# Performance work log

Measured on AMD Instinct MI355X. Metric: run time of the kernel, lower is better.

The kernel has to match this reference:

```python
import jax, jax.numpy as jnp
import numpy as np

N_NODES = 2048
EMBED = 256
STATE = 128
HID = 256
N_ACT = 256
TEAMS = 8
PAIR_F = 14


def setup_inputs() -> dict:
    key = jax.random.key(0)
    ks = jax.random.split(key, 12)
    B, T = 16, 32
    node_embeddings = jax.random.normal(ks[0], (N_NODES, EMBED), jnp.float32)
    states = jax.random.normal(ks[1], (B, T, STATE), jnp.float32)
    pair_features = jax.random.normal(ks[2], (B, T, N_ACT, PAIR_F), jnp.float32)
    proc_action_indices = jax.random.randint(ks[3], (N_ACT,), 0, N_NODES)
    in_dim = EMBED * 4 + PAIR_F
    s = lambda k, sh, fan: jax.random.normal(k, sh, jnp.float32) / np.sqrt(fan)
    return {
        "node_embeddings": node_embeddings,
        "states": states,
        "pair_features": pair_features,
        "proc_action_indices": proc_action_indices,
        "team_table": jax.random.normal(ks[4], (TEAMS, EMBED), jnp.float32),
        "Ws": s(ks[5], (STATE, EMBED), STATE),
        "bs": jnp.zeros((EMBED,), jnp.float32),
        "W1": s(ks[6], (in_dim, HID), in_dim),
        "b1": jnp.zeros((HID,), jnp.float32),
        "W2": s(ks[7], (HID, HID), HID),
        "b2": jnp.zeros((HID,), jnp.float32),
        "W3": s(ks[8], (HID, 1), HID),
        "b3": jnp.zeros((1,), jnp.float32),
    }


def reference(node_embeddings, states, pair_features, proc_action_indices,
              team_table, Ws, bs, W1, b1, W2, b2, W3, b3):
    B, T, A, F = pair_features.shape
    team_ids = jnp.arange(A) % TEAMS  # registered buffer
    # [A, E] gathered / per-action embeddings
    proc_emb = node_embeddings[proc_action_indices]          # [A, E]
    team_emb = team_table[team_ids]                          # [A, E]
    global_emb = jnp.mean(node_embeddings, axis=0)           # [E]
    state_emb = jax.nn.relu(states @ Ws + bs)                # [B, T, E]
    # broadcast + concat -> [B, T, A, 4E + F]
    bT = (B, T, A)
    scorer_input = jnp.concatenate([
        jnp.broadcast_to(proc_emb[None, None], bT + (proc_emb.shape[-1],)),
        jnp.broadcast_to(team_emb[None, None], bT + (team_emb.shape[-1],)),
        jnp.broadcast_to(global_emb[None, None, None], bT + (global_emb.shape[-1],)),
        jnp.broadcast_to(state_emb[:, :, None], bT + (state_emb.shape[-1],)),
        pair_features,
    ], axis=-1)
    h = jax.nn.relu(scorer_input @ W1 + b1)
    h = jax.nn.relu(h @ W2 + b2)
    scores = (h @ W3 + b3)[..., 0]  # [B, T, A]
    return scores[:, :, None, :]    # [B, T, 1, A]
```

## Files before the change

kernel.cpp:

```cpp
#include <hip/hip_runtime.h>
#include <hip/hip_bf16.h>

#define N_NODES 2048
#define EMBED 256
#define STATE 128
#define HID 256
#define N_ACT 256
#define TEAMS 8
#define PAIR_F 14
#define BT_TOTAL 512
#define M_TOTAL (BT_TOTAL * N_ACT)

typedef _Float16 f16_t;
typedef _Float16 f16x8 __attribute__((ext_vector_type(8)));
typedef _Float16 f16x4 __attribute__((ext_vector_type(4)));
typedef float f32x4 __attribute__((ext_vector_type(4)));

__device__ __forceinline__ size_t reord_idx(int k, int n, int KB) {
    return (size_t)(((n >> 4) * KB + (k >> 5)) * 4 + ((k >> 3) & 3)) * 128 +
           (size_t)(n & 15) * 8 + (k & 7);
}

__device__ __forceinline__ size_t par_idx(int a, int n) {
    return (size_t)(a >> 4) * 4096 + (size_t)(n >> 2) * 64 + (a & 15) * 4 + (n & 3);
}

__global__ void k_prep(const float* __restrict__ ne, const int* __restrict__ idx,
                       const float* __restrict__ team, const float* __restrict__ states,
                       const float* __restrict__ Ws, const float* __restrict__ W1,
                       const float* __restrict__ W2, float* __restrict__ gpart,
                       f16_t* __restrict__ vecs, f16_t* __restrict__ W1abT,
                       f16_t* __restrict__ W1dT, f16_t* __restrict__ WsT,
                       f16_t* __restrict__ W2s, f16_t* __restrict__ w1pt,
                       f16_t* __restrict__ states_h) {
    int bid = blockIdx.x;
    if (bid < 64) {
        int t = threadIdx.x;
        float s = 0.f;
        const float* base = ne + (size_t)bid * 32 * EMBED + t;
#pragma unroll
        for (int i = 0; i < 32; ++i) s += base[(size_t)i * EMBED];
        gpart[bid * EMBED + t] = s;
        return;
    }
    int i = (bid - 64) * 256 + threadIdx.x;
    if (i < 131072) {
        int a = i >> 9, e = i & 511;
        float v = (e < 256) ? ne[(size_t)idx[a] * EMBED + e]
                            : team[(a % TEAMS) * EMBED + (e - 256)];
        vecs[i] = (f16_t)v;
        return;
    }
    i -= 131072;
    if (i < 131072) {
        int k = i >> 8, n = i & 255;
        W1abT[reord_idx(k, n, 16)] = (f16_t)W1[(size_t)k * HID + n];
        return;
    }
    i -= 131072;
    if (i < 65536) {
        int k = i >> 8, n = i & 255;
        W1dT[reord_idx(k, n, 8)] = (f16_t)W1[(size_t)(768 + k) * HID + n];
        return;
    }
    i -= 65536;
    if (i < 32768) {
        int k = i >> 8, n = i & 255;
        WsT[reord_idx(k, n, 4)] = (f16_t)Ws[(size_t)k * EMBED + n];
        return;
    }
    i -= 32768;
    if (i < 65536) {
        int k = i >> 8, n = i & 255;
        W2s[reord_idx(k, n, 8)] = (f16_t)W2[(size_t)k * HID + n];
        return;
    }
    i -= 65536;
    if (i < 8192) {
        int k = i >> 8, n = i & 255;
        float v = (k < PAIR_F) ? W1[(size_t)(1024 + k) * HID + n] : 0.f;
        w1pt[reord_idx(k, n, 1)] = (f16_t)v;
        return;
    }
    i -= 8192;
    if (i < 65536) states_h[i] = (f16_t)states[i];
}

__global__ __launch_bounds__(256, 4) void k_pp(
    const f16_t* __restrict__ states_h, const f16_t* __restrict__ WsT,
    const float* __restrict__ bs, const f16_t* __restrict__ W1dT,
    const f16_t* __restrict__ vecs, const f16_t* __restrict__ W1abT,
    const float* __restrict__ W1, const float* __restrict__ b1,
    const float* __restrict__ gpart, f16_t* __restrict__ paR,
    f16_t* __restrict__ pbt_h) {
    __shared__ __align__(16) f16_t se[64 * 256];
    __shared__ float gm[256];
    const int tid = threadIdx.x;
    const int wid = tid >> 6, lane = tid & 63;
    const int c = lane & 15, q = lane >> 4;
    int bid = blockIdx.x;

    if (bid >= 8) {
        int b = bid - 8;
        const int m0 = (b >> 2) * 64, n0 = (b & 3) * 64;
        const int n = n0 + wid * 16 + c;
        const int g = n >> 4;
        f32x4 acc[4] = {f32x4{0,0,0,0}, f32x4{0,0,0,0}, f32x4{0,0,0,0}, f32x4{0,0,0,0}};
        for (int ks = 0; ks < 16; ++ks) {
            f16x8 bf = *(const f16x8*)(W1abT + (size_t)((g * 16 + ks) * 4 + q) * 128 + c * 8);
#pragma unroll
            for (int mi = 0; mi < 4; ++mi) {
                f16x8 af = *(const f16x8*)(vecs + (size_t)(m0 + mi * 16 + c) * 512 + ks * 32 + q * 8);
                acc[mi] = __builtin_amdgcn_mfma_f32_16x16x32_f16(af, bf, acc[mi], 0, 0, 0);
            }
        }
        {
            float s = 0.f;
#pragma unroll 8
            for (int p = 0; p < 64; ++p) s += gpart[p * EMBED + tid];
            gm[tid] = s * (1.0f / N_NODES);
        }
        __syncthreads();
        float cvec = 0.f;
#pragma unroll 8
        for (int e = 0; e < 256; ++e)
            cvec = fmaf(gm[e], W1[(size_t)(512 + e) * HID + n], cvec);
        cvec += b1[n];
#pragma unroll
        for (int mi = 0; mi < 4; ++mi)
#pragma unroll
            for (int j = 0; j < 4; ++j) {
                int a = m0 + mi * 16 + q * 4 + j;
                paR[par_idx(a, n)] = (f16_t)(acc[mi][j] + cvec);
            }
        return;
    }

    const int bt0 = bid * 64;
    f32x4 acc[4][4];
#pragma unroll
    for (int mi = 0; mi < 4; ++mi)
#pragma unroll
        for (int ni = 0; ni < 4; ++ni) acc[mi][ni] = f32x4{0, 0, 0, 0};
#pragma unroll
    for (int ks = 0; ks < 4; ++ks) {
        f16x8 bh[4];
#pragma unroll
        for (int ni = 0; ni < 4; ++ni) {
            int g = wid * 4 + ni;
            bh[ni] = *(const f16x8*)(WsT + (size_t)((g * 4 + ks) * 4 + q) * 128 + c * 8);
        }
#pragma unroll
        for (int mi = 0; mi < 4; ++mi) {
            f16x8 af = *(const f16x8*)(states_h + (size_t)(bt0 + mi * 16 + c) * STATE + ks * 32 + q * 8);
#pragma unroll
            for (int ni = 0; ni < 4; ++ni)
                acc[mi][ni] = __builtin_amdgcn_mfma_f32_16x16x32_f16(af, bh[ni], acc[mi][ni], 0, 0, 0);
        }
    }
#pragma unroll
    for (int mi = 0; mi < 4; ++mi)
#pragma unroll
        for (int ni = 0; ni < 4; ++ni) {
            float bsv = bs[wid * 64 + ni * 16 + c];
#pragma unroll
            for (int j = 0; j < 4; ++j) {
                int m = mi * 16 + q * 4 + j;
                int n = wid * 64 + ni * 16 + c;
                se[m * 256 + (n ^ ((m & 7) << 3))] = (f16_t)fmaxf(acc[mi][ni][j] + bsv, 0.f);
            }
        }
#pragma unroll
    for (int mi = 0; mi < 4; ++mi)
#pragma unroll
        for (int ni = 0; ni < 4; ++ni) acc[mi][ni] = f32x4{0, 0, 0, 0};
    __syncthreads();
#pragma unroll
    for (int ks = 0; ks < 8; ++ks) {
        f16x8 bh[4];
#pragma unroll
        for (int ni = 0; ni < 4; ++ni) {
            int g = wid * 4 + ni;
            bh[ni] = *(const f16x8*)(W1dT + (size_t)((g * 8 + ks) * 4 + q) * 128 + c * 8);
        }
#pragma unroll
        for (int mi = 0; mi < 4; ++mi) {
            int m = mi * 16 + c;
            f16x8 ah = *(const f16x8*)(&se[m * 256 + ((ks * 32 + q * 8) ^ ((m & 7) << 3))]);
#pragma unroll
            for (int ni = 0; ni < 4; ++ni)
                acc[mi][ni] = __builtin_amdgcn_mfma_f32_16x16x32_f16(ah, bh[ni], acc[mi][ni], 0, 0, 0);
        }
    }
#pragma unroll
    for (int mi = 0; mi < 4; ++mi)
#pragma unroll
        for (int ni = 0; ni < 4; ++ni)
#pragma unroll
            for (int j = 0; j < 4; ++j)
                pbt_h[(size_t)(bt0 + mi * 16 + q * 4 + j) * HID + wid * 64 + ni * 16 + c] =
                    (f16_t)acc[mi][ni][j];
}

__global__ __launch_bounds__(256, 4) void k_main(
    const float* __restrict__ pf, const f16_t* __restrict__ paR,
    const f16_t* __restrict__ pbt, const f16_t* __restrict__ w2s,
    const f16_t* __restrict__ w1pt, const float* __restrict__ b2,
    const float* __restrict__ W3, const float* __restrict__ b3,
    float* __restrict__ out) {
    __shared__ __align__(16) f16_t Ah[64 * 256];
    __shared__ float red[4][64];

    const int tid = threadIdx.x;
    const int wc = tid >> 6, lane = tid & 63;
    const int c = lane & 15, q = lane >> 4;

    const int r0 = blockIdx.x * 64;
    const int bt = r0 >> 8;
    const int a0 = r0 & 255;

    f32x4 acc[16];
#pragma unroll
    for (int i = 0; i < 16; ++i) acc[i] = f32x4{0, 0, 0, 0};

    f16x8 af[4];
#pragma unroll
    for (int nf = 0; nf < 4; ++nf) {
        int g = wc * 4 + nf;
        af[nf] = *(const f16x8*)(w1pt + (size_t)(g * 4 + q) * 128 + c * 8);
    }
#pragma unroll
    for (int mf = 0; mf < 4; ++mf) {
        int m = mf * 16 + c;
        const float* row = pf + (size_t)(r0 + m) * PAIR_F;
        float2 v01{0, 0}, v23{0, 0}, v45{0, 0}, v67{0, 0};
        if (q == 0) {
            v01 = *(const float2*)(row);
            v23 = *(const float2*)(row + 2);
            v45 = *(const float2*)(row + 4);
            v67 = *(const float2*)(row + 6);
        } else if (q == 1) {
            v01 = *(const float2*)(row + 8);
            v23 = *(const float2*)(row + 10);
            v45 = *(const float2*)(row + 12);
        }
        f16x8 bf;
        bf[0] = (f16_t)v01.x; bf[1] = (f16_t)v01.y;
        bf[2] = (f16_t)v23.x; bf[3] = (f16_t)v23.y;
        bf[4] = (f16_t)v45.x; bf[5] = (f16_t)v45.y;
        bf[6] = (f16_t)v67.x; bf[7] = (f16_t)v67.y;
#pragma unroll
        for (int nf = 0; nf < 4; ++nf)
            acc[nf * 4 + mf] = __builtin_amdgcn_mfma_f32_16x16x32_f16(af[nf], bf, acc[nf * 4 + mf], 0, 0, 0);
    }

#pragma unroll
    for (int nf = 0; nf < 4; ++nf) {
        int n0 = wc * 64 + nf * 16 + q * 4;
        f16x4 pbtv = *(const f16x4*)(pbt + (size_t)bt * HID + n0);
#pragma unroll
        for (int mf = 0; mf < 4; ++mf) {
            int m = mf * 16 + c;
            f16x4 pav = *(const f16x4*)(paR + (size_t)((a0 >> 4) + mf) * 4096 +
                                        (size_t)(n0 >> 2) * 64 + c * 4);
            f16x4 hv;
#pragma unroll
            for (int j = 0; j < 4; ++j) {
                float h = acc[nf * 4 + mf][j] + (float)pav[j] + (float)pbtv[j];
                hv[j] = (f16_t)fmaxf(h, 0.f);
            }
            *(f16x4*)(&Ah[m * 256 + (n0 ^ ((m & 7) << 3))]) = hv;
        }
    }

#pragma unroll
    for (int i = 0; i < 16; ++i) acc[i] = f32x4{0, 0, 0, 0};

    __syncthreads();

#pragma unroll
    for (int ks = 0; ks < 8; ++ks) {
        f16x8 bh[4];
#pragma unroll
        for (int ni = 0; ni < 4; ++ni) {
            int g = wc * 4 + ni;
            bh[ni] = *(const f16x8*)(w2s + (size_t)((g * 8 + ks) * 4 + q) * 128 + c * 8);
        }
#pragma unroll
        for (int mi = 0; mi < 4; ++mi) {
            int m = mi * 16 + c;
            int kx = (ks * 32 + q * 8) ^ ((m & 7) << 3);
            f16x8 ah = *(const f16x8*)(&Ah[m * 256 + kx]);
#pragma unroll
            for (int ni = 0; ni < 4; ++ni)
                acc[mi * 4 + ni] = __builtin_amdgcn_mfma_f32_16x16x32_f16(ah, bh[ni], acc[mi * 4 + ni], 0, 0, 0);
        }
    }

    float p[4][4];
#pragma unroll
    for (int mi = 0; mi < 4; ++mi)
#pragma unroll
        for (int j = 0; j < 4; ++j) p[mi][j] = 0.f;
#pragma unroll
    for (int ni = 0; ni < 4; ++ni) {
        int n = wc * 64 + ni * 16 + c;
        float b2v = b2[n];
        float w3v = W3[n];
#pragma unroll
        for (int mi = 0; mi < 4; ++mi)
#pragma unroll
            for (int j = 0; j < 4; ++j)
                p[mi][j] = fmaf(fmaxf(acc[mi * 4 + ni][j] + b2v, 0.f), w3v, p[mi][j]);
    }
#pragma unroll
    for (int off = 1; off < 16; off <<= 1)
#pragma unroll
        for (int mi = 0; mi < 4; ++mi)
#pragma unroll
            for (int j = 0; j < 4; ++j) p[mi][j] += __shfl_xor(p[mi][j], off, 64);

    if (c == 0) {
#pragma unroll
        for (int mi = 0; mi < 4; ++mi)
#pragma unroll
            for (int j = 0; j < 4; ++j) red[wc][mi * 16 + q * 4 + j] = p[mi][j];
    }
    __syncthreads();

    if (tid < 64) {
        out[(size_t)r0 + tid] = red[0][tid] + red[1][tid] + red[2][tid] + red[3][tid] + b3[0];
    }
}

extern "C" void kernel_launch(void* const* d_in, const int* in_sizes, int n_in,
                              void* d_out, int out_size, void* d_ws, size_t ws_size,
                              hipStream_t stream) {
    (void)in_sizes; (void)n_in; (void)out_size; (void)ws_size;
    const float* ne     = (const float*)d_in[0];
    const float* states = (const float*)d_in[1];
    const float* pf     = (const float*)d_in[2];
    const int*   idx    = (const int*)d_in[3];
    const float* team   = (const float*)d_in[4];
    const float* Ws     = (const float*)d_in[5];
    const float* bs     = (const float*)d_in[6];
    const float* W1     = (const float*)d_in[7];
    const float* b1     = (const float*)d_in[8];
    const float* W2     = (const float*)d_in[9];
    const float* b2     = (const float*)d_in[10];
    const float* W3     = (const float*)d_in[11];
    const float* b3     = (const float*)d_in[12];
    float* out = (float*)d_out;

    char* ws = (char*)d_ws;
    float* gpart    = (float*)(ws + 0);
    f16_t* vecs     = (f16_t*)(ws + 65536);
    f16_t* W1abT    = (f16_t*)(ws + 327680);
    f16_t* W1dT     = (f16_t*)(ws + 589824);
    f16_t* WsT      = (f16_t*)(ws + 720896);
    f16_t* W2s      = (f16_t*)(ws + 786432);
    f16_t* w1pt     = (f16_t*)(ws + 917504);
    f16_t* states_h = (f16_t*)(ws + 933888);
    f16_t* paR      = (f16_t*)(ws + 1064960);
    f16_t* pbt_h    = (f16_t*)(ws + 1196032);

    k_prep<<<64 + 1952, 256, 0, stream>>>(ne, idx, team, states, Ws, W1, W2,
                                          gpart, vecs, W1abT, W1dT, WsT, W2s, w1pt, states_h);
    k_pp<<<24, 256, 0, stream>>>(states_h, WsT, bs, W1dT, vecs, W1abT, W1, b1,
                                 gpart, paR, pbt_h);
    k_main<<<M_TOTAL / 64, 256, 0, stream>>>(pf, paR, pbt_h, W2s, w1pt, b2, W3, b3, out);
}
```

Before: 52.98 us.

## Split global-mean into own kernel, MFMA the mean projection, stage pair features in LDS

The global-mean column sums move into a separate small kernel. k_prep then finishes the mean as fp16 and converts the W1 global-embedding block, so k_pp computes the constant term with MFMA instead of a serial 256-step scalar dot product per thread. k_main loads the block's pair features with coalesced float4 loads into shared memory and double-buffers the W2 fragment loads across k-steps. The costs are an extra kernel launch, an extra barrier in k_main, and the mean projection now running in fp16.

```diff
diff --git a/kernel.cpp b/kernel.cpp
--- a/kernel.cpp
+++ b/kernel.cpp
@@ -25,25 +25,26 @@
     return (size_t)(a >> 4) * 4096 + (size_t)(n >> 2) * 64 + (a & 15) * 4 + (n & 3);
 }
 
+__global__ void k_cs(const float* __restrict__ ne, float* __restrict__ gpart) {
+    int b = blockIdx.x;
+    int t = threadIdx.x;
+    float s = 0.f;
+    const float* base = ne + (size_t)b * 32 * EMBED + t;
+#pragma unroll
+    for (int i = 0; i < 32; ++i) s += base[(size_t)i * EMBED];
+    gpart[b * EMBED + t] = s;
+}
+
 __global__ void k_prep(const float* __restrict__ ne, const int* __restrict__ idx,
                        const float* __restrict__ team, const float* __restrict__ states,
                        const float* __restrict__ Ws, const float* __restrict__ W1,
-                       const float* __restrict__ W2, float* __restrict__ gpart,
+                       const float* __restrict__ W2, const float* __restrict__ gpart,
                        f16_t* __restrict__ vecs, f16_t* __restrict__ W1abT,
-                       f16_t* __restrict__ W1dT, f16_t* __restrict__ WsT,
-                       f16_t* __restrict__ W2s, f16_t* __restrict__ w1pt,
-                       f16_t* __restrict__ states_h) {
-    int bid = blockIdx.x;
-    if (bid < 64) {
-        int t = threadIdx.x;
-        float s = 0.f;
-        const float* base = ne + (size_t)bid * 32 * EMBED + t;
-#pragma unroll
-        for (int i = 0; i < 32; ++i) s += base[(size_t)i * EMBED];
-        gpart[bid * EMBED + t] = s;
-        return;
-    }
-    int i = (bid - 64) * 256 + threadIdx.x;
+                       f16_t* __restrict__ W1cT, f16_t* __restrict__ W1dT,
+                       f16_t* __restrict__ WsT, f16_t* __restrict__ W2s,
+                       f16_t* __restrict__ w1pt, f16_t* __restrict__ states_h,
+                       f16_t* __restrict__ gm_h) {
+    int i = blockIdx.x * 256 + threadIdx.x;
     if (i < 131072) {
         int a = i >> 9, e = i & 511;
         float v = (e < 256) ? ne[(size_t)idx[a] * EMBED + e]
@@ -60,6 +61,12 @@
     i -= 131072;
     if (i < 65536) {
         int k = i >> 8, n = i & 255;
+        W1cT[reord_idx(k, n, 8)] = (f16_t)W1[(size_t)(512 + k) * HID + n];
+        return;
+    }
+    i -= 65536;
+    if (i < 65536) {
+        int k = i >> 8, n = i & 255;
         W1dT[reord_idx(k, n, 8)] = (f16_t)W1[(size_t)(768 + k) * HID + n];
         return;
     }
@@ -83,18 +90,24 @@
         return;
     }
     i -= 8192;
-    if (i < 65536) states_h[i] = (f16_t)states[i];
+    if (i < 65536) { states_h[i] = (f16_t)states[i]; return; }
+    i -= 65536;
+    if (i < 256) {
+        float s = 0.f;
+#pragma unroll 8
+        for (int p = 0; p < 64; ++p) s += gpart[p * EMBED + i];
+        gm_h[i] = (f16_t)(s * (1.0f / N_NODES));
+    }
 }
 
 __global__ __launch_bounds__(256, 4) void k_pp(
     const f16_t* __restrict__ states_h, const f16_t* __restrict__ WsT,
     const float* __restrict__ bs, const f16_t* __restrict__ W1dT,
     const f16_t* __restrict__ vecs, const f16_t* __restrict__ W1abT,
-    const float* __restrict__ W1, const float* __restrict__ b1,
-    const float* __restrict__ gpart, f16_t* __restrict__ paR,
+    const f16_t* __restrict__ W1cT, const f16_t* __restrict__ gm_h,
+    const float* __restrict__ b1, f16_t* __restrict__ paR,
     f16_t* __restrict__ pbt_h) {
     __shared__ __align__(16) f16_t se[64 * 256];
-    __shared__ float gm[256];
     const int tid = threadIdx.x;
     const int wid = tid >> 6, lane = tid & 63;
     const int c = lane & 15, q = lane >> 4;
@@ -114,24 +127,21 @@
                 acc[mi] = __builtin_amdgcn_mfma_f32_16x16x32_f16(af, bf, acc[mi], 0, 0, 0);
             }
         }
-        {
-            float s = 0.f;
-#pragma unroll 8
-            for (int p = 0; p < 64; ++p) s += gpart[p * EMBED + tid];
-            gm[tid] = s * (1.0f / N_NODES);
-        }
-        __syncthreads();
-        float cvec = 0.f;
-#pragma unroll 8
-        for (int e = 0; e < 256; ++e)
-            cvec = fmaf(gm[e], W1[(size_t)(512 + e) * HID + n], cvec);
-        cvec += b1[n];
+#pragma unroll
+        for (int ks = 0; ks < 8; ++ks) {
+            f16x8 bf = *(const f16x8*)(W1cT + (size_t)((g * 8 + ks) * 4 + q) * 128 + c * 8);
+            f16x8 af = *(const f16x8*)(gm_h + ks * 32 + q * 8);
+#pragma unroll
+            for (int mi = 0; mi < 4; ++mi)
+                acc[mi] = __builtin_amdgcn_mfma_f32_16x16x32_f16(af, bf, acc[mi], 0, 0, 0);
+        }
+        float b1v = b1[n];
 #pragma unroll
         for (int mi = 0; mi < 4; ++mi)
 #pragma unroll
             for (int j = 0; j < 4; ++j) {
                 int a = m0 + mi * 16 + q * 4 + j;
-                paR[par_idx(a, n)] = (f16_t)(acc[mi][j] + cvec);
+                paR[par_idx(a, n)] = (f16_t)(acc[mi][j] + b1v);
             }
         return;
     }
@@ -209,6 +219,7 @@
     const float* __restrict__ W3, const float* __restrict__ b3,
     float* __restrict__ out) {
     __shared__ __align__(16) f16_t Ah[64 * 256];
+    __shared__ __align__(16) float pfs[64 * PAIR_F];
     __shared__ float red[4][64];
 
     const int tid = threadIdx.x;
@@ -219,6 +230,11 @@
     const int bt = r0 >> 8;
     const int a0 = r0 & 255;
 
+    if (tid < 224) {
+        const float4 v = ((const float4*)(pf + (size_t)r0 * PAIR_F))[tid];
+        *(float4*)&pfs[tid * 4] = v;
+    }
+
     f32x4 acc[16];
 #pragma unroll
     for (int i = 0; i < 16; ++i) acc[i] = f32x4{0, 0, 0, 0};
@@ -229,26 +245,19 @@
         int g = wc * 4 + nf;
         af[nf] = *(const f16x8*)(w1pt + (size_t)(g * 4 + q) * 128 + c * 8);
     }
+
+    __syncthreads();
+
 #pragma unroll
     for (int mf = 0; mf < 4; ++mf) {
         int m = mf * 16 + c;
-        const float* row = pf + (size_t)(r0 + m) * PAIR_F;
-        float2 v01{0, 0}, v23{0, 0}, v45{0, 0}, v67{0, 0};
-        if (q == 0) {
-            v01 = *(const float2*)(row);
-            v23 = *(const float2*)(row + 2);
-            v45 = *(const float2*)(row + 4);
-            v67 = *(const float2*)(row + 6);
-        } else if (q == 1) {
-            v01 = *(const float2*)(row + 8);
-            v23 = *(const float2*)(row + 10);
-            v45 = *(const float2*)(row + 12);
-        }
         f16x8 bf;
-        bf[0] = (f16_t)v01.x; bf[1] = (f16_t)v01.y;
-        bf[2] = (f16_t)v23.x; bf[3] = (f16_t)v23.y;
-        bf[4] = (f16_t)v45.x; bf[5] = (f16_t)v45.y;
-        bf[6] = (f16_t)v67.x; bf[7] = (f16_t)v67.y;
+#pragma unroll
+        for (int j = 0; j < 8; ++j) {
+            int k = q * 8 + j;
+            float v = (q < 2 && k < PAIR_F) ? pfs[m * PAIR_F + k] : 0.f;
+            bf[j] = (f16_t)v;
+        }
 #pragma unroll
         for (int nf = 0; nf < 4; ++nf)
             acc[nf * 4 + mf] = __builtin_amdgcn_mfma_f32_16x16x32_f16(af[nf], bf, acc[nf * 4 + mf], 0, 0, 0);
@@ -278,13 +287,21 @@
 
     __syncthreads();
 
+    f16x8 bh[4];
+#pragma unroll
+    for (int ni = 0; ni < 4; ++ni) {
+        int g = wc * 4 + ni;
+        bh[ni] = *(const f16x8*)(w2s + (size_t)((g * 8 + 0) * 4 + q) * 128 + c * 8);
+    }
 #pragma unroll
     for (int ks = 0; ks < 8; ++ks) {
-        f16x8 bh[4];
-#pragma unroll
-        for (int ni = 0; ni < 4; ++ni) {
-            int g = wc * 4 + ni;
-            bh[ni] = *(const f16x8*)(w2s + (size_t)((g * 8 + ks) * 4 + q) * 128 + c * 8);
+        f16x8 bhn[4];
+        if (ks < 7) {
+#pragma unroll
+            for (int ni = 0; ni < 4; ++ni) {
+                int g = wc * 4 + ni;
+                bhn[ni] = *(const f16x8*)(w2s + (size_t)((g * 8 + ks + 1) * 4 + q) * 128 + c * 8);
+            }
         }
 #pragma unroll
         for (int mi = 0; mi < 4; ++mi) {
@@ -295,6 +312,8 @@
             for (int ni = 0; ni < 4; ++ni)
                 acc[mi * 4 + ni] = __builtin_amdgcn_mfma_f32_16x16x32_f16(ah, bh[ni], acc[mi * 4 + ni], 0, 0, 0);
         }
+#pragma unroll
+        for (int ni = 0; ni < 4; ++ni) bh[ni] = bhn[ni];
     }
 
     float p[4][4];
@@ -356,17 +375,21 @@
     float* gpart    = (float*)(ws + 0);
     f16_t* vecs     = (f16_t*)(ws + 65536);
     f16_t* W1abT    = (f16_t*)(ws + 327680);
-    f16_t* W1dT     = (f16_t*)(ws + 589824);
-    f16_t* WsT      = (f16_t*)(ws + 720896);
-    f16_t* W2s      = (f16_t*)(ws + 786432);
-    f16_t* w1pt     = (f16_t*)(ws + 917504);
-    f16_t* states_h = (f16_t*)(ws + 933888);
-    f16_t* paR      = (f16_t*)(ws + 1064960);
-    f16_t* pbt_h    = (f16_t*)(ws + 1196032);
-
-    k_prep<<<64 + 1952, 256, 0, stream>>>(ne, idx, team, states, Ws, W1, W2,
-                                          gpart, vecs, W1abT, W1dT, WsT, W2s, w1pt, states_h);
-    k_pp<<<24, 256, 0, stream>>>(states_h, WsT, bs, W1dT, vecs, W1abT, W1, b1,
-                                 gpart, paR, pbt_h);
+    f16_t* W1cT     = (f16_t*)(ws + 589824);
+    f16_t* W1dT     = (f16_t*)(ws + 720896);
+    f16_t* WsT      = (f16_t*)(ws + 851968);
+    f16_t* W2s      = (f16_t*)(ws + 917504);
+    f16_t* w1pt     = (f16_t*)(ws + 1048576);
+    f16_t* states_h = (f16_t*)(ws + 1064960);
+    f16_t* gm_h     = (f16_t*)(ws + 1196032);
+    f16_t* paR      = (f16_t*)(ws + 1196544);
+    f16_t* pbt_h    = (f16_t*)(ws + 1327616);
+
+    k_cs<<<64, 256, 0, stream>>>(ne, gpart);
+    k_prep<<<2209, 256, 0, stream>>>(ne, idx, team, states, Ws, W1, W2, gpart,
+                                     vecs, W1abT, W1cT, W1dT, WsT, W2s, w1pt,
+                                     states_h, gm_h);
+    k_pp<<<24, 256, 0, stream>>>(states_h, WsT, bs, W1dT, vecs, W1abT, W1cT,
+                                 gm_h, b1, paR, pbt_h);
     k_main<<<M_TOTAL / 64, 256, 0, stream>>>(pf, paR, pbt_h, W2s, w1pt, b2, W3, b3, out);
 }
```

After: 51.85 us. -2.1%, faster.
